# Performance work log

Hardware: AMD Instinct MI355X
Metric: run time of the kernel (lower is better)

The kernel has to match this reference:

```python
import jax, jax.numpy as jnp
import numpy as np

N = 8192
IN_F = 512
OUT_F = 64
ALPHA = 0.2   # LeakyReLU negative slope
STDV = 0.2
NEG_INF = -9e15


def setup_inputs() -> dict:
    key = jax.random.key(0)
    k1, k2, k3, k4 = jax.random.split(key, 4)
    x = jax.random.normal(k1, (N, IN_F), dtype=jnp.float32)
    adj = jax.random.randint(k2, (N, N), 0, 2, dtype=jnp.int32)
    W = jax.random.normal(k3, (IN_F, OUT_F), dtype=jnp.float32) * STDV
    a = jax.random.normal(k4, (2 * OUT_F, 1), dtype=jnp.float32) * STDV
    return {"x": x, "adj": adj, "W": W, "a": a}


def reference(x, adj, W, a):
    # Wh: [N, F']
    Wh = x @ W
    # attention logits: e[i,j] = leakyrelu(Wh[i]@a1 + Wh[j]@a2)
    Wh1 = Wh @ a[:OUT_F, :]   # [N, 1]
    Wh2 = Wh @ a[OUT_F:, :]   # [N, 1]
    e = Wh1 + Wh2.T           # [N, N] via broadcast
    e = jnp.where(e >= 0, e, ALPHA * e)  # LeakyReLU
    # mask by adjacency, row softmax
    masked = jnp.where(adj > 0, e, jnp.float32(NEG_INF))
    attention = jax.nn.softmax(masked, axis=1)
    # dropout rate is 0.0 in this config -> identity
    h_prime = attention @ Wh  # [N, F']
    out = jnp.where(h_prime > 0, h_prime, jnp.expm1(h_prime))  # ELU
    return out, attention
```

## Files before the change

kernel.cpp:

```cpp
#include <hip/hip_runtime.h>
#include <cmath>

#define Nn    8192
#define INF_  512
#define OUTF  64

typedef __attribute__((ext_vector_type(4))) int   i4;
typedef __attribute__((ext_vector_type(4))) float f4v;
typedef __attribute__((ext_vector_type(8))) short s8;
typedef __attribute__((ext_vector_type(4))) float f32x4;
typedef unsigned long long u64;

__device__ __forceinline__ float lrelu(float v) { return fmaxf(v, 0.2f * v); }

__device__ __forceinline__ unsigned int f2bf(float f) {
    unsigned int u = __float_as_uint(f);
    u = (u + 0x7FFFu + ((u >> 16) & 1u)) >> 16;
    return u;
}

__global__ __launch_bounds__(1024, 8) void k1_wh(
    const float* __restrict__ x, const float* __restrict__ W,
    const float* __restrict__ a, unsigned short* __restrict__ WhT,
    float* __restrict__ Wh1, float* __restrict__ Wh2)
{
    __shared__ float xs[16][520];
    __shared__ float part[3][16][64];
    __shared__ unsigned short stage[64][16];
    const int t    = threadIdx.x;
    const int row0 = blockIdx.x * 16;

    #pragma unroll
    for (int s2 = 0; s2 < 2; ++s2) {
        const int idx = s2 * 4096 + 4 * t;
        const f4v v = __builtin_nontemporal_load(
            (const f4v*)(x + (size_t)row0 * INF_ + idx));
        *(f4v*)&xs[idx >> 9][idx & 511] = v;
    }
    __syncthreads();

    const int s    = t >> 8;
    const int r    = (t >> 4) & 15;
    const int cg   = (t & 15) << 2;
    const int row  = row0 + r;
    const float* __restrict__ Wp = W + (size_t)s * 128 * OUTF;

    float4 acc = make_float4(0.f, 0.f, 0.f, 0.f);
    for (int k = 0; k < 128; k += 4) {
        const float4 xv = *(const float4*)&xs[r][s * 128 + k];
        const float* wp = Wp + (size_t)k * OUTF + cg;
        const float4 w0 = *(const float4*)(wp);
        const float4 w1 = *(const float4*)(wp + OUTF);
        const float4 w2 = *(const float4*)(wp + 2 * OUTF);
        const float4 w3 = *(const float4*)(wp + 3 * OUTF);
        acc.x += xv.x * w0.x + xv.y * w1.x + xv.z * w2.x + xv.w * w3.x;
        acc.y += xv.x * w0.y + xv.y * w1.y + xv.z * w2.y + xv.w * w3.y;
        acc.z += xv.x * w0.z + xv.y * w1.z + xv.z * w2.z + xv.w * w3.z;
        acc.w += xv.x * w0.w + xv.y * w1.w + xv.z * w2.w + xv.w * w3.w;
    }
    if (s > 0) *(float4*)&part[s - 1][r][cg] = acc;
    __syncthreads();
    if (s == 0) {
        const float4 pa = *(const float4*)&part[0][r][cg];
        const float4 pb = *(const float4*)&part[1][r][cg];
        const float4 pc = *(const float4*)&part[2][r][cg];
        acc.x += pa.x + pb.x + pc.x;
        acc.y += pa.y + pb.y + pc.y;
        acc.z += pa.z + pb.z + pc.z;
        acc.w += pa.w + pb.w + pc.w;
        stage[cg + 0][r] = (unsigned short)f2bf(acc.x);
        stage[cg + 1][r] = (unsigned short)f2bf(acc.y);
        stage[cg + 2][r] = (unsigned short)f2bf(acc.z);
        stage[cg + 3][r] = (unsigned short)f2bf(acc.w);

        float p1 = acc.x * a[cg]        + acc.y * a[cg + 1]
                 + acc.z * a[cg + 2]    + acc.w * a[cg + 3];
        float p2 = acc.x * a[OUTF + cg]     + acc.y * a[OUTF + cg + 1]
                 + acc.z * a[OUTF + cg + 2] + acc.w * a[OUTF + cg + 3];
        #pragma unroll
        for (int off = 8; off; off >>= 1) {
            p1 += __shfl_xor(p1, off);
            p2 += __shfl_xor(p2, off);
        }
        if ((t & 15) == 0) { Wh1[row] = p1; Wh2[row] = p2; }
    }
    __syncthreads();
    if (t < 256) {
        const int col = t >> 2;
        const int q   = t & 3;
        const u64 v = *(const u64*)&stage[col][q * 4];
        *(u64*)(WhT + (size_t)col * Nn + row0 + q * 4) = v;
    }
}

__global__ __launch_bounds__(1024, 8) void k2_fused(
    const int* __restrict__ adj, const unsigned short* __restrict__ WhT,
    const float* __restrict__ Wh1, const float* __restrict__ Wh2,
    float* __restrict__ outp, float* __restrict__ att)
{
    __shared__ unsigned char bm8[16][2048];
    __shared__ alignas(16) unsigned short att_t[2][16 * 256];
    __shared__ float red[3][4][16][16];
    __shared__ float sm_Sp[16][16];
    __shared__ float sm_is[16];

    const int t    = threadIdx.x;
    const int lane = t & 63;
    const int w    = t >> 6;
    const int row0 = blockIdx.x * 16;

    {
        const i4* __restrict__ asrc = (const i4*)(adj + (size_t)row0 * Nn);
        const int j0 = 4 * t;
        const f4v w4a = *(const f4v*)(Wh2 + j0);
        const f4v w4b = *(const f4v*)(Wh2 + 4096 + j0);
        float Sp = 0.f;
        i4 av = __builtin_nontemporal_load(asrc + t);
        #pragma unroll
        for (int s = 0; s < 32; ++s) {
            const int r = s >> 1, h = s & 1;
            i4 nxt;
            if (s < 31)
                nxt = __builtin_nontemporal_load(asrc + (s + 1) * 1024 + t);
            const f4v w4 = h ? w4b : w4a;
            const float h1r = Wh1[row0 + r];
            const int nib = (av.x != 0 ? 1 : 0) | (av.y != 0 ? 2 : 0)
                          | (av.z != 0 ? 4 : 0) | (av.w != 0 ? 8 : 0);
            Sp += (nib & 1) ? __expf(lrelu(h1r + w4.x)) : 0.f;
            Sp += (nib & 2) ? __expf(lrelu(h1r + w4.y)) : 0.f;
            Sp += (nib & 4) ? __expf(lrelu(h1r + w4.z)) : 0.f;
            Sp += (nib & 8) ? __expf(lrelu(h1r + w4.w)) : 0.f;
            bm8[r][h * 1024 + t] = (unsigned char)nib;
            if (h) {
                #pragma unroll
                for (int off = 32; off; off >>= 1) Sp += __shfl_xor(Sp, off);
                if (lane == 0) sm_Sp[r][w] = Sp;
                Sp = 0.f;
            }
            av = nxt;
        }
    }
    __syncthreads();

    {
        float sv = sm_Sp[w][lane & 15];
        #pragma unroll
        for (int off = 8; off; off >>= 1) sv += __shfl_xor(sv, off);
        if (lane == 0) sm_is[w] = 1.0f / sv;
    }
    __syncthreads();

    const int row = row0 + w;
    const float h1 = Wh1[row];
    const float is = sm_is[w];

    const int ct = w & 3;
    const int kq = w >> 2;
    f32x4 acc = {0.f, 0.f, 0.f, 0.f};

    auto produce = [&](int c, int bf) {
        const int jb = c * 256;
        const f4v w2 = *((const f4v*)(Wh2 + jb) + lane);
        const int nib = bm8[w][c * 64 + lane];
        const float v0 = (nib & 1) ? __expf(lrelu(h1 + w2.x)) * is : 0.f;
        const float v1 = (nib & 2) ? __expf(lrelu(h1 + w2.y)) * is : 0.f;
        const float v2 = (nib & 4) ? __expf(lrelu(h1 + w2.z)) * is : 0.f;
        const float v3 = (nib & 8) ? __expf(lrelu(h1 + w2.w)) * is : 0.f;
        f4v st; st.x = v0; st.y = v1; st.z = v2; st.w = v3;
        __builtin_nontemporal_store(st, (f4v*)(att + (size_t)row * Nn + jb) + lane);
        const u64 pk = (u64)(f2bf(v0) | (f2bf(v1) << 16))
                     | ((u64)(f2bf(v2) | (f2bf(v3) << 16)) << 32);
        int byte = w * 512 + lane * 8;  byte ^= (w & 7) << 4;
        *(u64*)((char*)att_t[bf] + byte) = pk;
    };

    const int ar = lane & 15;
    const int ag = lane >> 4;
    auto bload = [&](int c, int ss) -> s8 {
        const int ks = kq * 2 + ss;
        return *(const s8*)(WhT + (size_t)(ct * 16 + ar) * Nn
                            + c * 256 + ks * 32 + ag * 8);
    };
    auto amfma = [&](int bf, s8 b0, s8 b1) {
        #pragma unroll
        for (int ss = 0; ss < 2; ++ss) {
            const int ks = kq * 2 + ss;
            int byte = ar * 512 + ks * 64 + ag * 16;
            byte ^= (ar & 7) << 4;
            const s8 af = *(const s8*)((char*)att_t[bf] + byte);
            acc = __builtin_amdgcn_mfma_f32_16x16x32_bf16(af, ss ? b1 : b0, acc, 0, 0, 0);
        }
    };

    s8 b0 = bload(0, 0), b1 = bload(0, 1);
    produce(0, 0);
    asm volatile("s_waitcnt lgkmcnt(0)" ::: "memory");
    __builtin_amdgcn_s_barrier();
    for (int c = 0; c < Nn / 256 - 1; ++c) {
        produce(c + 1, (c + 1) & 1);
        const s8 nb0 = bload(c + 1, 0);
        const s8 nb1 = bload(c + 1, 1);
        amfma(c & 1, b0, b1);
        asm volatile("s_waitcnt lgkmcnt(0)" ::: "memory");
        __builtin_amdgcn_s_barrier();
        b0 = nb0; b1 = nb1;
    }
    amfma((Nn / 256 - 1) & 1, b0, b1);

    __syncthreads();
    if (kq > 0) {
        #pragma unroll
        for (int q = 0; q < 4; ++q) red[kq - 1][ct][ag * 4 + q][ar] = acc[q];
    }
    __syncthreads();
    if (kq == 0) {
        #pragma unroll
        for (int q = 0; q < 4; ++q) {
            const int r = ag * 4 + q;
            float v = acc[q] + red[0][ct][r][ar] + red[1][ct][r][ar] + red[2][ct][r][ar];
            v = v > 0.f ? v : expm1f(v);
            outp[(size_t)(row0 + r) * OUTF + ct * 16 + ar] = v;
        }
    }
}

extern "C" void kernel_launch(void* const* d_in, const int* in_sizes, int n_in,
                              void* d_out, int out_size, void* d_ws, size_t ws_size,
                              hipStream_t stream)
{
    const float* x   = (const float*)d_in[0];
    const int*   adj = (const int*)d_in[1];
    const float* W   = (const float*)d_in[2];
    const float* a   = (const float*)d_in[3];

    float* outp = (float*)d_out;
    float* att  = outp + (size_t)Nn * OUTF;

    float* Wh1 = (float*)d_ws;
    float* Wh2 = Wh1 + Nn;
    unsigned short* WhT = (unsigned short*)(Wh2 + Nn);

    hipLaunchKernelGGL(k1_wh,    dim3(Nn / 16), dim3(1024), 0, stream,
                       x, W, a, WhT, Wh1, Wh2);
    hipLaunchKernelGGL(k2_fused, dim3(Nn / 16), dim3(1024), 0, stream,
                       adj, WhT, Wh1, Wh2, outp, att);
}
```

Measured before the change: 162.0 us.

## Split K across waves with register A fragments, drop LDS double buffer and barriers

The second phase now gives each of the 16 waves its own 512-column slice of K. Each wave computes attention values for all 16 rows directly into MFMA A-fragment registers and accumulates all four 16-column output tiles. This removes the LDS att_t staging buffer and the per-chunk block barriers. Partial results are combined with LDS atomicAdds at the end. The cost is scattered 32-byte att stores per lane instead of row-contiguous ones, and uncoalesced WhT loads without prefetch.

```diff
diff --git a/kernel.cpp b/kernel.cpp
--- a/kernel.cpp
+++ b/kernel.cpp
@@ -98,9 +98,8 @@
     const float* __restrict__ Wh1, const float* __restrict__ Wh2,
     float* __restrict__ outp, float* __restrict__ att)
 {
-    __shared__ unsigned char bm8[16][2048];
-    __shared__ alignas(16) unsigned short att_t[2][16 * 256];
-    __shared__ float red[3][4][16][16];
+    __shared__ unsigned char bm8[16][2064];
+    __shared__ float red[4][16][16];
     __shared__ float sm_Sp[16][16];
     __shared__ float sm_is[16];
 
@@ -109,11 +108,12 @@
     const int w    = t >> 6;
     const int row0 = blockIdx.x * 16;
 
+    const int j0 = 4 * t;
+    const f4v w4a = *(const f4v*)(Wh2 + j0);
+    const f4v w4b = *(const f4v*)(Wh2 + 4096 + j0);
+
     {
         const i4* __restrict__ asrc = (const i4*)(adj + (size_t)row0 * Nn);
-        const int j0 = 4 * t;
-        const f4v w4a = *(const f4v*)(Wh2 + j0);
-        const f4v w4b = *(const f4v*)(Wh2 + 4096 + j0);
         float Sp = 0.f;
         i4 av = __builtin_nontemporal_load(asrc + t);
         #pragma unroll
@@ -148,79 +148,79 @@
         for (int off = 8; off; off >>= 1) sv += __shfl_xor(sv, off);
         if (lane == 0) sm_is[w] = 1.0f / sv;
     }
-    __syncthreads();
-
-    const int row = row0 + w;
-    const float h1 = Wh1[row];
-    const float is = sm_is[w];
-
-    const int ct = w & 3;
-    const int kq = w >> 2;
-    f32x4 acc = {0.f, 0.f, 0.f, 0.f};
-
-    auto produce = [&](int c, int bf) {
-        const int jb = c * 256;
-        const f4v w2 = *((const f4v*)(Wh2 + jb) + lane);
-        const int nib = bm8[w][c * 64 + lane];
-        const float v0 = (nib & 1) ? __expf(lrelu(h1 + w2.x)) * is : 0.f;
-        const float v1 = (nib & 2) ? __expf(lrelu(h1 + w2.y)) * is : 0.f;
-        const float v2 = (nib & 4) ? __expf(lrelu(h1 + w2.z)) * is : 0.f;
-        const float v3 = (nib & 8) ? __expf(lrelu(h1 + w2.w)) * is : 0.f;
-        f4v st; st.x = v0; st.y = v1; st.z = v2; st.w = v3;
-        __builtin_nontemporal_store(st, (f4v*)(att + (size_t)row * Nn + jb) + lane);
-        const u64 pk = (u64)(f2bf(v0) | (f2bf(v1) << 16))
-                     | ((u64)(f2bf(v2) | (f2bf(v3) << 16)) << 32);
-        int byte = w * 512 + lane * 8;  byte ^= (w & 7) << 4;
-        *(u64*)((char*)att_t[bf] + byte) = pk;
-    };
-
-    const int ar = lane & 15;
-    const int ag = lane >> 4;
-    auto bload = [&](int c, int ss) -> s8 {
-        const int ks = kq * 2 + ss;
-        return *(const s8*)(WhT + (size_t)(ct * 16 + ar) * Nn
-                            + c * 256 + ks * 32 + ag * 8);
-    };
-    auto amfma = [&](int bf, s8 b0, s8 b1) {
-        #pragma unroll
-        for (int ss = 0; ss < 2; ++ss) {
-            const int ks = kq * 2 + ss;
-            int byte = ar * 512 + ks * 64 + ag * 16;
-            byte ^= (ar & 7) << 4;
-            const s8 af = *(const s8*)((char*)att_t[bf] + byte);
-            acc = __builtin_amdgcn_mfma_f32_16x16x32_bf16(af, ss ? b1 : b0, acc, 0, 0, 0);
-        }
-    };
-
-    s8 b0 = bload(0, 0), b1 = bload(0, 1);
-    produce(0, 0);
-    asm volatile("s_waitcnt lgkmcnt(0)" ::: "memory");
-    __builtin_amdgcn_s_barrier();
-    for (int c = 0; c < Nn / 256 - 1; ++c) {
-        produce(c + 1, (c + 1) & 1);
-        const s8 nb0 = bload(c + 1, 0);
-        const s8 nb1 = bload(c + 1, 1);
-        amfma(c & 1, b0, b1);
-        asm volatile("s_waitcnt lgkmcnt(0)" ::: "memory");
-        __builtin_amdgcn_s_barrier();
-        b0 = nb0; b1 = nb1;
-    }
-    amfma((Nn / 256 - 1) & 1, b0, b1);
-
-    __syncthreads();
-    if (kq > 0) {
-        #pragma unroll
-        for (int q = 0; q < 4; ++q) red[kq - 1][ct][ag * 4 + q][ar] = acc[q];
-    }
-    __syncthreads();
-    if (kq == 0) {
-        #pragma unroll
-        for (int q = 0; q < 4; ++q) {
-            const int r = ag * 4 + q;
-            float v = acc[q] + red[0][ct][r][ar] + red[1][ct][r][ar] + red[2][ct][r][ar];
-            v = v > 0.f ? v : expm1f(v);
-            outp[(size_t)(row0 + r) * OUTF + ct * 16 + ar] = v;
-        }
+    ((float*)red)[t] = 0.f;
+    __syncthreads();
+
+    const int brow = lane & 15;
+    const int kg   = lane >> 4;
+    const float h1r = Wh1[row0 + brow];
+    const float isr = sm_is[brow];
+    const size_t rowbase = (size_t)(row0 + brow) * Nn;
+
+    f32x4 a0 = {0.f,0.f,0.f,0.f}, a1 = {0.f,0.f,0.f,0.f};
+    f32x4 a2 = {0.f,0.f,0.f,0.f}, a3 = {0.f,0.f,0.f,0.f};
+
+    for (int ks = 0; ks < 16; ++ks) {
+        const int jb = w * 512 + ks * 32 + kg * 8;
+        const unsigned short nn = *(const unsigned short*)&bm8[brow][jb >> 2];
+        const int nib0 = nn & 0xFF;
+        const int nib1 = nn >> 8;
+        const f4v wa = *(const f4v*)(Wh2 + jb);
+        const f4v wb = *(const f4v*)(Wh2 + jb + 4);
+        const float v0 = (nib0 & 1) ? __expf(lrelu(h1r + wa.x)) * isr : 0.f;
+        const float v1 = (nib0 & 2) ? __expf(lrelu(h1r + wa.y)) * isr : 0.f;
+        const float v2 = (nib0 & 4) ? __expf(lrelu(h1r + wa.z)) * isr : 0.f;
+        const float v3 = (nib0 & 8) ? __expf(lrelu(h1r + wa.w)) * isr : 0.f;
+        const float v4 = (nib1 & 1) ? __expf(lrelu(h1r + wb.x)) * isr : 0.f;
+        const float v5 = (nib1 & 2) ? __expf(lrelu(h1r + wb.y)) * isr : 0.f;
+        const float v6 = (nib1 & 4) ? __expf(lrelu(h1r + wb.z)) * isr : 0.f;
+        const float v7 = (nib1 & 8) ? __expf(lrelu(h1r + wb.w)) * isr : 0.f;
+
+        f4v sa; sa.x = v0; sa.y = v1; sa.z = v2; sa.w = v3;
+        f4v sb; sb.x = v4; sb.y = v5; sb.z = v6; sb.w = v7;
+        __builtin_nontemporal_store(sa, (f4v*)(att + rowbase + jb));
+        __builtin_nontemporal_store(sb, (f4v*)(att + rowbase + jb + 4));
+
+        s8 af;
+        af[0] = (short)f2bf(v0); af[1] = (short)f2bf(v1);
+        af[2] = (short)f2bf(v2); af[3] = (short)f2bf(v3);
+        af[4] = (short)f2bf(v4); af[5] = (short)f2bf(v5);
+        af[6] = (short)f2bf(v6); af[7] = (short)f2bf(v7);
+
+        const unsigned short* __restrict__ wt = WhT + (size_t)brow * Nn + jb;
+        {
+            const s8 bf = *(const s8*)(wt);
+            a0 = __builtin_amdgcn_mfma_f32_16x16x32_bf16(af, bf, a0, 0, 0, 0);
+        }
+        {
+            const s8 bf = *(const s8*)(wt + (size_t)16 * Nn);
+            a1 = __builtin_amdgcn_mfma_f32_16x16x32_bf16(af, bf, a1, 0, 0, 0);
+        }
+        {
+            const s8 bf = *(const s8*)(wt + (size_t)32 * Nn);
+            a2 = __builtin_amdgcn_mfma_f32_16x16x32_bf16(af, bf, a2, 0, 0, 0);
+        }
+        {
+            const s8 bf = *(const s8*)(wt + (size_t)48 * Nn);
+            a3 = __builtin_amdgcn_mfma_f32_16x16x32_bf16(af, bf, a3, 0, 0, 0);
+        }
+    }
+
+    #pragma unroll
+    for (int q = 0; q < 4; ++q) {
+        atomicAdd(&red[0][kg * 4 + q][brow], a0[q]);
+        atomicAdd(&red[1][kg * 4 + q][brow], a1[q]);
+        atomicAdd(&red[2][kg * 4 + q][brow], a2[q]);
+        atomicAdd(&red[3][kg * 4 + q][brow], a3[q]);
+    }
+    __syncthreads();
+
+    {
+        const int r = t >> 6;
+        const int c = t & 63;
+        float v = red[c >> 4][r][c & 15];
+        v = v > 0.f ? v : expm1f(v);
+        outp[(size_t)(row0 + r) * OUTF + c] = v;
     }
 }
 
```

Result: slower. 189.4 us (+16.9%).

## Factor exp of LeakyReLU into precomputed per-node exponentials

Applied to the files above, without the earlier changes.

Uses exp(lrelu(a+b)) = exp(a)exp(b) when a+b>0 and exp(0.2a)exp(0.2b) otherwise. The per-node exponentials are computed once in the first kernel, so the N×N exp work in the fused kernel becomes a compare, a select and a multiply. Sign bits are packed next to the adjacency nibble in shared memory, and the bitmap row is padded. This adds four extra per-node arrays that are loaded per chunk, and products of exponentials may overflow or lose precision for large logits.

```diff
diff --git a/kernel.cpp b/kernel.cpp
--- a/kernel.cpp
+++ b/kernel.cpp
@@ -22,7 +22,9 @@
 __global__ __launch_bounds__(1024, 8) void k1_wh(
     const float* __restrict__ x, const float* __restrict__ W,
     const float* __restrict__ a, unsigned short* __restrict__ WhT,
-    float* __restrict__ Wh1, float* __restrict__ Wh2)
+    float* __restrict__ Wh1, float* __restrict__ Wh2,
+    float* __restrict__ e1g, float* __restrict__ e1qg,
+    float* __restrict__ e2g, float* __restrict__ e2qg)
 {
     __shared__ float xs[16][520];
     __shared__ float part[3][16][64];
@@ -82,7 +84,11 @@
             p1 += __shfl_xor(p1, off);
             p2 += __shfl_xor(p2, off);
         }
-        if ((t & 15) == 0) { Wh1[row] = p1; Wh2[row] = p2; }
+        if ((t & 15) == 0) {
+            Wh1[row] = p1;  Wh2[row] = p2;
+            e1g[row]  = __expf(p1);        e1qg[row] = __expf(0.2f * p1);
+            e2g[row]  = __expf(p2);        e2qg[row] = __expf(0.2f * p2);
+        }
     }
     __syncthreads();
     if (t < 256) {
@@ -96,9 +102,11 @@
 __global__ __launch_bounds__(1024, 8) void k2_fused(
     const int* __restrict__ adj, const unsigned short* __restrict__ WhT,
     const float* __restrict__ Wh1, const float* __restrict__ Wh2,
+    const float* __restrict__ e1g, const float* __restrict__ e1qg,
+    const float* __restrict__ e2g, const float* __restrict__ e2qg,
     float* __restrict__ outp, float* __restrict__ att)
 {
-    __shared__ unsigned char bm8[16][2048];
+    __shared__ unsigned char bm8[16][2064];
     __shared__ alignas(16) unsigned short att_t[2][16 * 256];
     __shared__ float red[3][4][16][16];
     __shared__ float sm_Sp[16][16];
@@ -109,12 +117,17 @@
     const int w    = t >> 6;
     const int row0 = blockIdx.x * 16;
 
+    const int j0 = 4 * t;
+    const f4v w4a  = *(const f4v*)(Wh2  + j0);
+    const f4v w4b  = *(const f4v*)(Wh2  + 4096 + j0);
+    const f4v e2a  = *(const f4v*)(e2g  + j0);
+    const f4v e2b  = *(const f4v*)(e2g  + 4096 + j0);
+    const f4v e2qa = *(const f4v*)(e2qg + j0);
+    const f4v e2qb = *(const f4v*)(e2qg + 4096 + j0);
+
     {
         const i4* __restrict__ asrc = (const i4*)(adj + (size_t)row0 * Nn);
-        const int j0 = 4 * t;
-        const f4v w4a = *(const f4v*)(Wh2 + j0);
-        const f4v w4b = *(const f4v*)(Wh2 + 4096 + j0);
-        float Sp = 0.f;
+        float Spp = 0.f, Spn = 0.f;
         i4 av = __builtin_nontemporal_load(asrc + t);
         #pragma unroll
         for (int s = 0; s < 32; ++s) {
@@ -122,20 +135,29 @@
             i4 nxt;
             if (s < 31)
                 nxt = __builtin_nontemporal_load(asrc + (s + 1) * 1024 + t);
-            const f4v w4 = h ? w4b : w4a;
-            const float h1r = Wh1[row0 + r];
+            const f4v w4  = h ? w4b  : w4a;
+            const f4v ev  = h ? e2b  : e2a;
+            const f4v evq = h ? e2qb : e2qa;
+            const float nh1 = -Wh1[row0 + r];
             const int nib = (av.x != 0 ? 1 : 0) | (av.y != 0 ? 2 : 0)
                           | (av.z != 0 ? 4 : 0) | (av.w != 0 ? 8 : 0);
-            Sp += (nib & 1) ? __expf(lrelu(h1r + w4.x)) : 0.f;
-            Sp += (nib & 2) ? __expf(lrelu(h1r + w4.y)) : 0.f;
-            Sp += (nib & 4) ? __expf(lrelu(h1r + w4.z)) : 0.f;
-            Sp += (nib & 8) ? __expf(lrelu(h1r + w4.w)) : 0.f;
-            bm8[r][h * 1024 + t] = (unsigned char)nib;
+            const int sgn = (w4.x > nh1 ? 1 : 0) | (w4.y > nh1 ? 2 : 0)
+                          | (w4.z > nh1 ? 4 : 0) | (w4.w > nh1 ? 8 : 0);
+            Spp += ((nib & sgn) & 1) ? ev.x  : 0.f;
+            Spn += ((nib & ~sgn) & 1) ? evq.x : 0.f;
+            Spp += ((nib & sgn) & 2) ? ev.y  : 0.f;
+            Spn += ((nib & ~sgn) & 2) ? evq.y : 0.f;
+            Spp += ((nib & sgn) & 4) ? ev.z  : 0.f;
+            Spn += ((nib & ~sgn) & 4) ? evq.z : 0.f;
+            Spp += ((nib & sgn) & 8) ? ev.w  : 0.f;
+            Spn += ((nib & ~sgn) & 8) ? evq.w : 0.f;
+            bm8[r][h * 1024 + t] = (unsigned char)(nib | (sgn << 4));
             if (h) {
+                float Sp = e1g[row0 + r] * Spp + e1qg[row0 + r] * Spn;
                 #pragma unroll
                 for (int off = 32; off; off >>= 1) Sp += __shfl_xor(Sp, off);
                 if (lane == 0) sm_Sp[r][w] = Sp;
-                Sp = 0.f;
+                Spp = 0.f; Spn = 0.f;
             }
             av = nxt;
         }
@@ -151,8 +173,9 @@
     __syncthreads();
 
     const int row = row0 + w;
-    const float h1 = Wh1[row];
-    const float is = sm_is[w];
+    const float is  = sm_is[w];
+    const float E1s  = e1g[row]  * is;
+    const float E1qs = e1qg[row] * is;
 
     const int ct = w & 3;
     const int kq = w >> 2;
@@ -160,12 +183,15 @@
 
     auto produce = [&](int c, int bf) {
         const int jb = c * 256;
-        const f4v w2 = *((const f4v*)(Wh2 + jb) + lane);
-        const int nib = bm8[w][c * 64 + lane];
-        const float v0 = (nib & 1) ? __expf(lrelu(h1 + w2.x)) * is : 0.f;
-        const float v1 = (nib & 2) ? __expf(lrelu(h1 + w2.y)) * is : 0.f;
-        const float v2 = (nib & 4) ? __expf(lrelu(h1 + w2.z)) * is : 0.f;
-        const float v3 = (nib & 8) ? __expf(lrelu(h1 + w2.w)) * is : 0.f;
+        const f4v ev  = *((const f4v*)(e2g  + jb) + lane);
+        const f4v evq = *((const f4v*)(e2qg + jb) + lane);
+        const int byte_ = bm8[w][c * 64 + lane];
+        const int nib = byte_ & 15;
+        const int sgn = byte_ >> 4;
+        const float v0 = (nib & 1) ? ((sgn & 1) ? E1s * ev.x : E1qs * evq.x) : 0.f;
+        const float v1 = (nib & 2) ? ((sgn & 2) ? E1s * ev.y : E1qs * evq.y) : 0.f;
+        const float v2 = (nib & 4) ? ((sgn & 4) ? E1s * ev.z : E1qs * evq.z) : 0.f;
+        const float v3 = (nib & 8) ? ((sgn & 8) ? E1s * ev.w : E1qs * evq.w) : 0.f;
         f4v st; st.x = v0; st.y = v1; st.z = v2; st.w = v3;
         __builtin_nontemporal_store(st, (f4v*)(att + (size_t)row * Nn + jb) + lane);
         const u64 pk = (u64)(f2bf(v0) | (f2bf(v1) << 16))
@@ -236,12 +262,16 @@
     float* outp = (float*)d_out;
     float* att  = outp + (size_t)Nn * OUTF;
 
-    float* Wh1 = (float*)d_ws;
-    float* Wh2 = Wh1 + Nn;
-    unsigned short* WhT = (unsigned short*)(Wh2 + Nn);
+    float* Wh1  = (float*)d_ws;
+    float* Wh2  = Wh1 + Nn;
+    float* e1g  = Wh2 + Nn;
+    float* e1qg = e1g + Nn;
+    float* e2g  = e1qg + Nn;
+    float* e2qg = e2g + Nn;
+    unsigned short* WhT = (unsigned short*)(e2qg + Nn);
 
     hipLaunchKernelGGL(k1_wh,    dim3(Nn / 16), dim3(1024), 0, stream,
-                       x, W, a, WhT, Wh1, Wh2);
+                       x, W, a, WhT, Wh1, Wh2, e1g, e1qg, e2g, e2qg);
     hipLaunchKernelGGL(k2_fused, dim3(Nn / 16), dim3(1024), 0, stream,
-                       adj, WhT, Wh1, Wh2, outp, att);
-}
+                       adj, WhT, Wh1, Wh2, e1g, e1qg, e2g, e2qg, outp, att);
+}
```

After: 169.9 us. 4.9% more time.
